# Optimization experiments

Hardware: AMD Instinct MI355X
Metric: run time of the kernel (lower is better)

## Reference

```python
import jax, jax.numpy as jnp
import numpy as np

B, T, D, H = 8, 1024, 768, 12
HD = D // H  # head_dim = 64


def setup_inputs() -> dict:
    key = jax.random.key(0)
    ks = jax.random.split(key, 6)
    s = 1.0 / np.sqrt(D)
    return {
        "x": jax.random.normal(ks[0], (B, T, D), dtype=jnp.float32),
        "Wq": jax.random.normal(ks[1], (D, D), dtype=jnp.float32) * s,
        "Wk": jax.random.normal(ks[2], (D, D), dtype=jnp.float32) * s,
        "Wv": jax.random.normal(ks[3], (D, D), dtype=jnp.float32) * s,
        "Wp": jax.random.normal(ks[4], (D, D), dtype=jnp.float32) * s,
        "bp": jnp.zeros((D,), dtype=jnp.float32),
    }


def reference(x, Wq, Wk, Wv, Wp, bp):
    Bx, Tx, Dx = x.shape
    # projections (nn.Linear applies x @ W.T; weights here are stored as [out,in]-equivalent square)
    q = (x @ Wq.T).reshape(Bx, Tx, H, HD).transpose(0, 2, 1, 3)  # [B,H,T,hd]
    k = (x @ Wk.T).reshape(Bx, Tx, H, HD).transpose(0, 2, 1, 3)
    v = (x @ Wv.T).reshape(Bx, Tx, H, HD).transpose(0, 2, 1, 3)
    scores = jnp.einsum("bhqd,bhkd->bhqk", q, k)  # raw QK^T, then mask, then scale (as in source)
    causal = jnp.tril(jnp.ones((Tx, Tx), dtype=bool))
    scores = jnp.where(causal, scores, -jnp.inf)
    weights = jax.nn.softmax(scores / np.sqrt(HD), axis=-1)
    # dropout is identity in eval mode
    ctx = jnp.einsum("bhqk,bhkd->bhqd", weights, v)
    ctx = ctx.transpose(0, 2, 1, 3).reshape(Bx, Tx, Dx)
    return ctx @ Wp.T + bp
```

## Files before the change

kernel.cpp:

```cpp
#include <hip/hip_runtime.h>
#include <hip/hip_bf16.h>
#include <math.h>

#define Bsz 8
#define Tsz 1024
#define Dsz 768
#define Hn  12
#define Msz (Bsz*Tsz)
#define NQT (Tsz/64)

typedef __attribute__((ext_vector_type(8))) short bf16x8_t;
typedef __attribute__((ext_vector_type(4))) float f32x4_t;

#define DPPF(v, CTRL) __builtin_bit_cast(float, __builtin_amdgcn_update_dpp( \
    0, __builtin_bit_cast(int, (v)), (CTRL), 0xF, 0xF, true))

__device__ __forceinline__ unsigned short f2bf(float f) {
  unsigned u = __builtin_bit_cast(unsigned, f);
  u += 0x7FFFu + ((u >> 16) & 1u);
  return (unsigned short)(u >> 16);
}

__device__ __forceinline__ unsigned short f2bf_fast(float f) {
  __hip_bfloat16 h = __float2bfloat16(f);
  return __builtin_bit_cast(unsigned short, h);
}

__device__ __forceinline__ void gload16(const void* g, const void* l) {
  __builtin_amdgcn_global_load_lds(
      (const __attribute__((address_space(1))) unsigned int*)g,
      (__attribute__((address_space(3))) unsigned int*)l, 16, 0, 0);
}

#define XBLKS (Msz*Dsz/1024)
#define WBLKS (Dsz*Dsz/1024)
__global__ __launch_bounds__(256) void cvt_all_kernel(
    const float* __restrict__ x,
    const float* __restrict__ w0, const float* __restrict__ w1,
    const float* __restrict__ w2, const float* __restrict__ w3,
    unsigned short* __restrict__ xb,
    unsigned short* __restrict__ o0, unsigned short* __restrict__ o1,
    unsigned short* __restrict__ o2, unsigned short* __restrict__ o3) {
  int bid = blockIdx.x;
  const float* src; unsigned short* dst; size_t blk;
  if (bid < XBLKS) { src = x; dst = xb; blk = bid; }
  else {
    int t = bid - XBLKS;
    int which = t / WBLKS;
    blk = t % WBLKS;
    switch (which) {
      case 0: src = w0; dst = o0; break;
      case 1: src = w1; dst = o1; break;
      case 2: src = w2; dst = o2; break;
      default: src = w3; dst = o3; break;
    }
  }
  size_t idx = (blk * 256 + threadIdx.x) * 4;
  float4 v = *(const float4*)(src + idx);
  union { unsigned short u[4]; uint2 w; } t;
  t.u[0] = f2bf(v.x); t.u[1] = f2bf(v.y); t.u[2] = f2bf(v.z); t.u[3] = f2bf(v.w);
  *(uint2*)(dst + idx) = t.w;
}

__global__ __launch_bounds__(256) void gemm_qkv_kernel(
    const unsigned short* __restrict__ X, const unsigned short* __restrict__ Wcat,
    unsigned short* __restrict__ Yq, unsigned short* __restrict__ Yk,
    unsigned short* __restrict__ Yvt) {
  __shared__ __align__(16) unsigned short As[128 * 64];
  __shared__ __align__(16) unsigned short Bs[128 * 64];
  const int tid = threadIdx.x;
  const int w = tid >> 6, lane = tid & 63;
  const int i = lane & 15, g = lane >> 4;
  const int wr = w >> 1, wc = w & 1;
  const int bm = blockIdx.x * 128, bn = blockIdx.y * 128;
  const int sr = lane >> 3;
  const int scb = ((lane & 7) * 16) ^ (sr << 4);

  f32x4_t acc[4][4];
  #pragma unroll
  for (int a = 0; a < 4; ++a)
    #pragma unroll
    for (int b2 = 0; b2 < 4; ++b2)
      #pragma unroll
      for (int r = 0; r < 4; ++r) acc[a][b2][r] = 0.f;

  for (int k0 = 0; k0 < Dsz; k0 += 64) {
    __syncthreads();
    #pragma unroll
    for (int j = 0; j < 4; ++j) {
      const int c = 4 * w + j;
      const int row = 8 * c + sr;
      gload16((const char*)X + ((size_t)(bm + row) * Dsz + k0) * 2 + scb,
              (const char*)As + c * 1024);
      gload16((const char*)Wcat + ((size_t)(bn + row) * Dsz + k0) * 2 + scb,
              (const char*)Bs + c * 1024);
    }
    __syncthreads();
    bf16x8_t af[4][2];
    #pragma unroll
    for (int f = 0; f < 4; ++f) {
      const int R = 64 * wr + 16 * f + i;
      #pragma unroll
      for (int kk = 0; kk < 2; ++kk)
        af[f][kk] = *(const bf16x8_t*)((const char*)As + R * 128 +
                                       ((64 * kk + 16 * g) ^ ((i & 7) << 4)));
    }
    #pragma unroll
    for (int b2 = 0; b2 < 4; ++b2) {
      const int R = 64 * wc + 16 * b2 + i;
      const bf16x8_t b0 = *(const bf16x8_t*)((const char*)Bs + R * 128 +
                                             ((16 * g) ^ ((i & 7) << 4)));
      const bf16x8_t b1 = *(const bf16x8_t*)((const char*)Bs + R * 128 +
                                             ((64 + 16 * g) ^ ((i & 7) << 4)));
      #pragma unroll
      for (int a = 0; a < 4; ++a) {
        acc[a][b2] = __builtin_amdgcn_mfma_f32_16x16x32_bf16(af[a][0], b0, acc[a][b2], 0, 0, 0);
        acc[a][b2] = __builtin_amdgcn_mfma_f32_16x16x32_bf16(af[a][1], b1, acc[a][b2], 0, 0, 0);
      }
    }
  }

  const int wsel = blockIdx.y / 6;
  const int nloc = (blockIdx.y % 6) * 128;
  if (wsel < 2) {
    unsigned short* Y = wsel ? Yk : Yq;
    const float sc = wsel ? 1.0f : 0.18033688f;
    #pragma unroll
    for (int fi = 0; fi < 4; ++fi)
      #pragma unroll
      for (int fj = 0; fj < 4; ++fj) {
        const int n = nloc + 64 * wc + 16 * fj + i;
        #pragma unroll
        for (int r = 0; r < 4; ++r) {
          const int m = bm + 64 * wr + 16 * fi + 4 * g + r;
          Y[(size_t)m * Dsz + n] = f2bf_fast(acc[fi][fj][r] * sc);
        }
      }
  } else {
    #pragma unroll
    for (int fi = 0; fi < 4; ++fi)
      #pragma unroll
      for (int fj = 0; fj < 4; ++fj) {
        const int m0 = bm + 64 * wr + 16 * fi + 4 * g;
        const int bb = m0 >> 10;
        const int t  = m0 & 1023;
        const int n  = nloc + 64 * wc + 16 * fj + i;
        union { unsigned short u[4]; uint2 v; } pk;
        #pragma unroll
        for (int r = 0; r < 4; ++r) pk.u[r] = f2bf_fast(acc[fi][fj][r]);
        *(uint2*)&Yvt[((size_t)(bb * Dsz + n)) * Tsz + t] = pk.v;
      }
  }
}

__global__ __launch_bounds__(256) void gemm_proj_kernel(
    const unsigned short* __restrict__ X, const unsigned short* __restrict__ W,
    const float* __restrict__ bias, float* __restrict__ Y) {
  __shared__ __align__(16) unsigned short As[128 * 64];
  __shared__ __align__(16) unsigned short Bs[128 * 64];
  const int tid = threadIdx.x;
  const int w = tid >> 6, lane = tid & 63;
  const int i = lane & 15, g = lane >> 4;
  const int wr = w >> 1, wc = w & 1;
  const int bm = blockIdx.x * 128, bn = blockIdx.y * 128;
  const int sr = lane >> 3;
  const int scb = ((lane & 7) * 16) ^ (sr << 4);

  f32x4_t acc[4][4];
  #pragma unroll
  for (int a = 0; a < 4; ++a)
    #pragma unroll
    for (int b2 = 0; b2 < 4; ++b2)
      #pragma unroll
      for (int r = 0; r < 4; ++r) acc[a][b2][r] = 0.f;

  for (int k0 = 0; k0 < Dsz; k0 += 64) {
    __syncthreads();
    #pragma unroll
    for (int j = 0; j < 4; ++j) {
      const int c = 4 * w + j;
      const int row = 8 * c + sr;
      gload16((const char*)X + ((size_t)(bm + row) * Dsz + k0) * 2 + scb,
              (const char*)As + c * 1024);
      gload16((const char*)W + ((size_t)(bn + row) * Dsz + k0) * 2 + scb,
              (const char*)Bs + c * 1024);
    }
    __syncthreads();
    bf16x8_t af[4][2];
    #pragma unroll
    for (int f = 0; f < 4; ++f) {
      const int R = 64 * wr + 16 * f + i;
      #pragma unroll
      for (int kk = 0; kk < 2; ++kk)
        af[f][kk] = *(const bf16x8_t*)((const char*)As + R * 128 +
                                       ((64 * kk + 16 * g) ^ ((i & 7) << 4)));
    }
    #pragma unroll
    for (int b2 = 0; b2 < 4; ++b2) {
      const int R = 64 * wc + 16 * b2 + i;
      const bf16x8_t b0 = *(const bf16x8_t*)((const char*)Bs + R * 128 +
                                             ((16 * g) ^ ((i & 7) << 4)));
      const bf16x8_t b1 = *(const bf16x8_t*)((const char*)Bs + R * 128 +
                                             ((64 + 16 * g) ^ ((i & 7) << 4)));
      #pragma unroll
      for (int a = 0; a < 4; ++a) {
        acc[a][b2] = __builtin_amdgcn_mfma_f32_16x16x32_bf16(af[a][0], b0, acc[a][b2], 0, 0, 0);
        acc[a][b2] = __builtin_amdgcn_mfma_f32_16x16x32_bf16(af[a][1], b1, acc[a][b2], 0, 0, 0);
      }
    }
  }

  #pragma unroll
  for (int fi = 0; fi < 4; ++fi)
    #pragma unroll
    for (int fj = 0; fj < 4; ++fj) {
      const int n = bn + 64 * wc + 16 * fj + i;
      const float bv = bias[n];
      #pragma unroll
      for (int r = 0; r < 4; ++r) {
        const int m = bm + 64 * wr + 16 * fi + 4 * g + r;
        Y[(size_t)m * Dsz + n] = acc[fi][fj][r] + bv;
      }
    }
}

__global__ __launch_bounds__(512) void attn_mfma_kernel(
    const unsigned short* __restrict__ Qm, const unsigned short* __restrict__ Km,
    const unsigned short* __restrict__ Vt, unsigned short* __restrict__ ctx) {
  __shared__ __align__(16) unsigned short Ks[2][64 * 64];
  __shared__ __align__(16) unsigned short Vs[2][64 * 64];
  __shared__ __align__(16) unsigned short Ps[8][16 * 72];
  const int tid = threadIdx.x, w = tid >> 6, lane = tid & 63;
  const int i = lane & 15, g = lane >> 4;
  const int grp = w >> 2, wl = w & 3;
  const int bh = blockIdx.x, b = bh / Hn, h = bh % Hn;
  const int j = blockIdx.y;
  const int qt = grp ? (NQT - 1 - j) : j;
  const int t0 = qt * 64;
  const int nkt = NQT - j;

  const int sr  = lane >> 3;
  const int swz = ((lane & 7) * 16) ^ (sr << 4);

  bf16x8_t qa[2];
  {
    const unsigned short* qp =
        Qm + ((size_t)(b * Tsz + t0 + 16 * wl + i) * Dsz + h * 64 + 8 * g);
    qa[0] = *(const bf16x8_t*)qp;
    qa[1] = *(const bf16x8_t*)(qp + 32);
  }

  f32x4_t o[4];
  #pragma unroll
  for (int fd = 0; fd < 4; ++fd)
    #pragma unroll
    for (int r = 0; r < 4; ++r) o[fd][r] = 0.f;
  float mrun[4] = {-3.0e38f, -3.0e38f, -3.0e38f, -3.0e38f};
  float lrun[4] = {0.f, 0.f, 0.f, 0.f};

  auto STAGE = [&](int kv0, int p) {
    const int row = 8 * w + sr;
    gload16((const char*)Km + ((size_t)(b * Tsz + kv0 + row) * Dsz + h * 64) * 2 + swz,
            (const char*)Ks[p] + w * 1024);
    gload16((const char*)Vt + ((size_t)(bh * 64 + row) * Tsz + kv0) * 2 + swz,
            (const char*)Vs[p] + w * 1024);
  };

  STAGE(0, 0);
  unsigned short* Pw = &Ps[w][0];

  for (int kt = 0; kt < nkt; ++kt) {
    const int p = kt & 1;
    __syncthreads();
    if (kt + 1 < nkt) STAGE((kt + 1) * 64, p ^ 1);

    if (kt <= qt) {
      f32x4_t s[4];
      __builtin_amdgcn_s_setprio(1);
      #pragma unroll
      for (int fj = 0; fj < 4; ++fj) {
        #pragma unroll
        for (int r = 0; r < 4; ++r) s[fj][r] = 0.f;
        const int R = 16 * fj + i;
        #pragma unroll
        for (int ks = 0; ks < 2; ++ks) {
          const bf16x8_t kb = *(const bf16x8_t*)((const char*)Ks[p] + R * 128 +
                                                 ((64 * ks + 16 * g) ^ ((i & 7) << 4)));
          s[fj] = __builtin_amdgcn_mfma_f32_16x16x32_bf16(qa[ks], kb, s[fj], 0, 0, 0);
        }
      }
      __builtin_amdgcn_s_setprio(0);

      if (kt == qt) {
        #pragma unroll
        for (int fj = 0; fj < 4; ++fj) {
          const int kidx = kt * 64 + 16 * fj + i;
          #pragma unroll
          for (int r = 0; r < 4; ++r)
            if (kidx > t0 + 16 * wl + 4 * g + r) s[fj][r] = -1.0e30f;
        }
      }

      float mx[4];
      #pragma unroll
      for (int r = 0; r < 4; ++r) {
        float v = fmaxf(fmaxf(s[0][r], s[1][r]), fmaxf(s[2][r], s[3][r]));
        v = fmaxf(v, DPPF(v, 0xB1));
        v = fmaxf(v, DPPF(v, 0x4E));
        v = fmaxf(v, DPPF(v, 0x141));
        v = fmaxf(v, DPPF(v, 0x140));
        mx[r] = v;
      }

      bool nd = false;
      #pragma unroll
      for (int r = 0; r < 4; ++r) nd = nd || (mx[r] > mrun[r] + 8.0f);
      if (__any(nd)) {
        #pragma unroll
        for (int r = 0; r < 4; ++r) {
          const float mn = fmaxf(mrun[r], mx[r]);
          const float fs = exp2f(mrun[r] - mn);
          mrun[r] = mn;
          lrun[r] *= fs;
          #pragma unroll
          for (int fd = 0; fd < 4; ++fd) o[fd][r] *= fs;
        }
      }

      #pragma unroll
      for (int fj = 0; fj < 4; ++fj)
        #pragma unroll
        for (int r = 0; r < 4; ++r) {
          s[fj][r] = exp2f(s[fj][r] - mrun[r]);
          lrun[r] += s[fj][r];
        }

      #pragma unroll
      for (int fj = 0; fj < 4; ++fj)
        #pragma unroll
        for (int r = 0; r < 4; ++r)
          Pw[(4 * g + r) * 72 + 16 * fj + i] = f2bf_fast(s[fj][r]);

      __builtin_amdgcn_s_setprio(1);
      #pragma unroll
      for (int ks = 0; ks < 2; ++ks) {
        const bf16x8_t pa = *(const bf16x8_t*)&Pw[i * 72 + 32 * ks + 8 * g];
        #pragma unroll
        for (int fd = 0; fd < 4; ++fd) {
          const int R = 16 * fd + i;
          const bf16x8_t vb = *(const bf16x8_t*)((const char*)Vs[p] + R * 128 +
                                                 ((64 * ks + 16 * g) ^ ((i & 7) << 4)));
          o[fd] = __builtin_amdgcn_mfma_f32_16x16x32_bf16(pa, vb, o[fd], 0, 0, 0);
        }
      }
      __builtin_amdgcn_s_setprio(0);
    }
  }

  #pragma unroll
  for (int r = 0; r < 4; ++r) {
    float l = lrun[r];
    l += DPPF(l, 0xB1);
    l += DPPF(l, 0x4E);
    l += DPPF(l, 0x141);
    l += DPPF(l, 0x140);
    const float inv = 1.f / l;
    const int qidx = t0 + 16 * wl + 4 * g + r;
    #pragma unroll
    for (int fd = 0; fd < 4; ++fd)
      ctx[(size_t)(b * Tsz + qidx) * Dsz + h * 64 + 16 * fd + i] =
          f2bf_fast(o[fd][r] * inv);
  }
}

extern "C" void kernel_launch(void* const* d_in, const int* in_sizes, int n_in,
                              void* d_out, int out_size, void* d_ws, size_t ws_size,
                              hipStream_t stream) {
  const float* x  = (const float*)d_in[0];
  const float* Wq = (const float*)d_in[1];
  const float* Wk = (const float*)d_in[2];
  const float* Wv = (const float*)d_in[3];
  const float* Wp = (const float*)d_in[4];
  const float* bp = (const float*)d_in[5];
  float* out = (float*)d_out;

  const size_t md = (size_t)Msz * Dsz;
  const size_t wd = (size_t)Dsz * Dsz;
  unsigned short* xb   = (unsigned short*)d_ws;
  unsigned short* wqb  = xb + md;
  unsigned short* wkb  = wqb + wd;
  unsigned short* wvb  = wkb + wd;
  unsigned short* wpb  = wvb + wd;
  unsigned short* qb   = wpb + wd;
  unsigned short* kb   = qb + md;
  unsigned short* vtb  = kb + md;
  unsigned short* ctxb = vtb + md;

  cvt_all_kernel<<<XBLKS + 4 * WBLKS, 256, 0, stream>>>(
      x, Wq, Wk, Wv, Wp, xb, wqb, wkb, wvb, wpb);

  gemm_qkv_kernel<<<dim3(Msz / 128, 18), 256, 0, stream>>>(xb, wqb, qb, kb, vtb);

  attn_mfma_kernel<<<dim3(Bsz * Hn, 8), 512, 0, stream>>>(qb, kb, vtb, ctxb);

  gemm_proj_kernel<<<dim3(Msz / 128, Dsz / 128), 256, 0, stream>>>(ctxb, wpb, bp, out);
}
```

Measured before the change: 202.2 us.

## Stage V-transpose epilogue through LDS and shrink proj GEMM tile to 128x64

The QKV GEMM's V output is now transposed through a swizzled shared-memory buffer, so each thread writes 16-byte rows to the [B,D,T] layout instead of scattered 8-byte stores. The projection GEMM tile drops from 128x128 to 128x64, doubling the grid from 384 to 768 blocks to fill the GPU better, with each wave now owning a 32x64 subtile. The smaller tile reuses each A tile less and reloads the activation operand more often. The LDS staging also adds two barriers to the V epilogue.

```diff
diff --git a/kernel.cpp b/kernel.cpp
--- a/kernel.cpp
+++ b/kernel.cpp
@@ -66,8 +66,9 @@
     const unsigned short* __restrict__ X, const unsigned short* __restrict__ Wcat,
     unsigned short* __restrict__ Yq, unsigned short* __restrict__ Yk,
     unsigned short* __restrict__ Yvt) {
-  __shared__ __align__(16) unsigned short As[128 * 64];
-  __shared__ __align__(16) unsigned short Bs[128 * 64];
+  __shared__ __align__(16) unsigned short SMEM[2 * 128 * 64];
+  unsigned short* As = SMEM;
+  unsigned short* Bs = SMEM + 128 * 64;
   const int tid = threadIdx.x;
   const int w = tid >> 6, lane = tid & 63;
   const int i = lane & 15, g = lane >> 4;
@@ -137,19 +138,30 @@
         }
       }
   } else {
+    __syncthreads();
     #pragma unroll
     for (int fi = 0; fi < 4; ++fi)
       #pragma unroll
       for (int fj = 0; fj < 4; ++fj) {
-        const int m0 = bm + 64 * wr + 16 * fi + 4 * g;
-        const int bb = m0 >> 10;
-        const int t  = m0 & 1023;
-        const int n  = nloc + 64 * wc + 16 * fj + i;
-        union { unsigned short u[4]; uint2 v; } pk;
-        #pragma unroll
-        for (int r = 0; r < 4; ++r) pk.u[r] = f2bf_fast(acc[fi][fj][r]);
-        *(uint2*)&Yvt[((size_t)(bb * Dsz + n)) * Tsz + t] = pk.v;
-      }
+        const int n_l = 64 * wc + 16 * fj + i;
+        #pragma unroll
+        for (int r = 0; r < 4; ++r) {
+          const int t_l = 64 * wr + 16 * fi + 4 * g + r;
+          SMEM[n_l * 128 + (t_l ^ ((n_l & 7) << 3))] = f2bf_fast(acc[fi][fj][r]);
+        }
+      }
+    __syncthreads();
+    const int n_r = tid >> 1;
+    const int th  = (tid & 1) * 64;
+    const int n_g = nloc + n_r;
+    const int bb  = bm >> 10;
+    const int tb  = bm & 1023;
+    #pragma unroll
+    for (int tc = 0; tc < 8; ++tc) {
+      const int t_l = th + tc * 8;
+      const uint4 v = *(const uint4*)&SMEM[n_r * 128 + (t_l ^ ((n_r & 7) << 3))];
+      *(uint4*)&Yvt[((size_t)(bb * Dsz + n_g)) * Tsz + tb + t_l] = v;
+    }
   }
 }
 
@@ -157,18 +169,17 @@
     const unsigned short* __restrict__ X, const unsigned short* __restrict__ W,
     const float* __restrict__ bias, float* __restrict__ Y) {
   __shared__ __align__(16) unsigned short As[128 * 64];
-  __shared__ __align__(16) unsigned short Bs[128 * 64];
+  __shared__ __align__(16) unsigned short Bs[64 * 64];
   const int tid = threadIdx.x;
   const int w = tid >> 6, lane = tid & 63;
   const int i = lane & 15, g = lane >> 4;
-  const int wr = w >> 1, wc = w & 1;
-  const int bm = blockIdx.x * 128, bn = blockIdx.y * 128;
+  const int bm = blockIdx.x * 128, bn = blockIdx.y * 64;
   const int sr = lane >> 3;
   const int scb = ((lane & 7) * 16) ^ (sr << 4);
 
-  f32x4_t acc[4][4];
+  f32x4_t acc[2][4];
   #pragma unroll
-  for (int a = 0; a < 4; ++a)
+  for (int a = 0; a < 2; ++a)
     #pragma unroll
     for (int b2 = 0; b2 < 4; ++b2)
       #pragma unroll
@@ -182,14 +193,19 @@
       const int row = 8 * c + sr;
       gload16((const char*)X + ((size_t)(bm + row) * Dsz + k0) * 2 + scb,
               (const char*)As + c * 1024);
+    }
+    #pragma unroll
+    for (int j = 0; j < 2; ++j) {
+      const int c = 2 * w + j;
+      const int row = 8 * c + sr;
       gload16((const char*)W + ((size_t)(bn + row) * Dsz + k0) * 2 + scb,
               (const char*)Bs + c * 1024);
     }
     __syncthreads();
-    bf16x8_t af[4][2];
-    #pragma unroll
-    for (int f = 0; f < 4; ++f) {
-      const int R = 64 * wr + 16 * f + i;
+    bf16x8_t af[2][2];
+    #pragma unroll
+    for (int f = 0; f < 2; ++f) {
+      const int R = 32 * w + 16 * f + i;
       #pragma unroll
       for (int kk = 0; kk < 2; ++kk)
         af[f][kk] = *(const bf16x8_t*)((const char*)As + R * 128 +
@@ -197,13 +213,13 @@
     }
     #pragma unroll
     for (int b2 = 0; b2 < 4; ++b2) {
-      const int R = 64 * wc + 16 * b2 + i;
+      const int R = 16 * b2 + i;
       const bf16x8_t b0 = *(const bf16x8_t*)((const char*)Bs + R * 128 +
                                              ((16 * g) ^ ((i & 7) << 4)));
       const bf16x8_t b1 = *(const bf16x8_t*)((const char*)Bs + R * 128 +
                                              ((64 + 16 * g) ^ ((i & 7) << 4)));
       #pragma unroll
-      for (int a = 0; a < 4; ++a) {
+      for (int a = 0; a < 2; ++a) {
         acc[a][b2] = __builtin_amdgcn_mfma_f32_16x16x32_bf16(af[a][0], b0, acc[a][b2], 0, 0, 0);
         acc[a][b2] = __builtin_amdgcn_mfma_f32_16x16x32_bf16(af[a][1], b1, acc[a][b2], 0, 0, 0);
       }
@@ -211,14 +227,14 @@
   }
 
   #pragma unroll
-  for (int fi = 0; fi < 4; ++fi)
+  for (int fi = 0; fi < 2; ++fi)
     #pragma unroll
     for (int fj = 0; fj < 4; ++fj) {
-      const int n = bn + 64 * wc + 16 * fj + i;
+      const int n = bn + 16 * fj + i;
       const float bv = bias[n];
       #pragma unroll
       for (int r = 0; r < 4; ++r) {
-        const int m = bm + 64 * wr + 16 * fi + 4 * g + r;
+        const int m = bm + 32 * w + 16 * fi + 4 * g + r;
         Y[(size_t)m * Dsz + n] = acc[fi][fj][r] + bv;
       }
     }
@@ -403,5 +419,5 @@
 
   attn_mfma_kernel<<<dim3(Bsz * Hn, 8), 512, 0, stream>>>(qb, kb, vtb, ctxb);
 
-  gemm_proj_kernel<<<dim3(Msz / 128, Dsz / 128), 256, 0, stream>>>(ctxb, wpb, bp, out);
-}
+  gemm_proj_kernel<<<dim3(Msz / 128, Dsz / 64), 256, 0, stream>>>(ctxb, wpb, bp, out);
+}
```

Measured after the change: 200.4 us. No clear change (-0.9%).
